# Kernel tuning notes

Hardware: AMD Instinct MI355X
Metric: run time of the kernel (lower is better)

The kernel has to match this reference:

```python
import jax, jax.numpy as jnp
import numpy as np
import math

N = 4096
E = 131072
D_IN = 148      # d_node_feat
D_HID = 128     # d_node_reshape (DIHGNN.d_node_feat)
D_OUT = 148     # d_output


def setup_inputs() -> dict:
    key = jax.random.key(0)
    ks = jax.random.split(key, 10)
    node_feat = jax.random.normal(ks[0], (1, N, D_IN), dtype=jnp.float32)
    edge_index = jax.random.randint(ks[1], (2, E), 0, N, dtype=jnp.int64)
    # learned parameters
    W1 = jax.random.normal(ks[2], (D_HID, D_IN), dtype=jnp.float32) * 0.02
    b1 = jnp.zeros((D_HID,), dtype=jnp.float32)
    a_param = jnp.array([0.9], dtype=jnp.float32)   # DIHGNN.a
    Wd = jax.random.normal(ks[3], (D_OUT, D_HID), dtype=jnp.float32) * 0.02
    bd = jnp.zeros((D_OUT,), dtype=jnp.float32)
    W2 = jax.random.normal(ks[4], (2, D_OUT), dtype=jnp.float32) * 0.02
    b2 = jnp.zeros((2,), dtype=jnp.float32)
    return {"node_feat": node_feat, "edge_index": edge_index, "num_node": N,
            "W1": W1, "b1": b1, "a_param": a_param, "Wd": Wd, "bd": bd,
            "W2": W2, "b2": b2}


def reference(node_feat, edge_index, num_node, W1, b1, a_param, Wd, bd, W2, b2):
    n = num_node
    x = node_feat[0]                                   # [N, D_IN]
    x = x @ W1.T + b1                                  # linear_1 -> [N, D_HID]

    # dense adjacency via scatter-set (duplicates collapse to 1, as in torch)
    adj = jnp.zeros((n, n), dtype=jnp.float32).at[edge_index[0], edge_index[1]].set(1.0)

    # asymmetric degree normalization: D_col^{-1/2} A D_row^{-1/2}
    L = adj.sum(axis=0)                                # column sums
    R = adj.sum(axis=1)                                # row sums
    L_is = jnp.where(L > 0, jax.lax.rsqrt(jnp.maximum(L, 1e-30)), 0.0)
    R_is = jnp.where(R > 0, jax.lax.rsqrt(jnp.maximum(R, 1e-30)), 0.0)
    adj_norm = L_is[:, None] * adj * R_is[None, :]

    # custom tanh: 0.5 + 0.5 * tanh(2 * a)
    alpha = 0.5 + 0.5 * jnp.tanh(2.0 * a_param[0])     # scalar

    # graph diffusion: (I - alpha * A_norm)^{-1} x, as a linear solve
    eye = jnp.eye(n, dtype=jnp.float32)
    x = jnp.linalg.solve(eye - alpha * adj_norm, x)    # [N, D_HID]

    x = x @ Wd.T + bd                                  # DIHGNN.linear -> [N, D_OUT]

    # similarity loss (scaled by DIHGNN.d_node_feat = D_HID)
    sim = (x @ x.T) / math.sqrt(D_HID)                 # [N, N]
    sim = sim * (1.0 - eye)                            # zero diagonal
    sim = jax.nn.relu(sim)
    loss = sim.sum() / (n * (n - 1))

    x = x * (1.0 - alpha)
    x = jax.nn.relu(x)
    pooled = jnp.max(x, axis=0, keepdims=True)         # global_max_pool, single graph -> [1, D_OUT]
    out = pooled @ W2.T + b2                           # [1, 2]
    return (out, loss)
```

## Files before the change

### kernel.cpp

```cpp
#include <hip/hip_runtime.h>
#include <hip/hip_bf16.h>
#include <math.h>

#define N_NODES 4096
#define N_EDGES 131072
#define BCAP 80
#define DIN 148
#define DHID 128
#define DOUT 148
#define KP 160

typedef __attribute__((ext_vector_type(8))) _Float16 half8;
typedef __attribute__((ext_vector_type(4))) float f32x4;

__device__ inline float2 h2f2(unsigned p) {
    union { unsigned u; _Float16 h[2]; } cv; cv.u = p;
    return make_float2((float)cv.h[0], (float)cv.h[1]);
}
__device__ inline unsigned f2h2(float x, float y) {
    union { unsigned u; _Float16 h[2]; } cv;
    cv.h[0] = (_Float16)x; cv.h[1] = (_Float16)y;
    return cv.u;
}
__device__ inline float2 cvtx(unsigned g) { return h2f2(g); }
__device__ inline float2 cvtx(float2 g)   { return g; }

__global__ __launch_bounds__(256) void prep_kernel(const int* __restrict__ ei,
                                                   const float* __restrict__ W1,
                                                   const float* __restrict__ Wd,
                                                   const float* __restrict__ b1,
                                                   const float* __restrict__ nf,
                                                   float* __restrict__ WdT,
                                                   unsigned* __restrict__ bitmap,
                                                   unsigned* __restrict__ bucket,
                                                   int* __restrict__ rowdeg,
                                                   int* __restrict__ coldeg,
                                                   float* __restrict__ Bm,
                                                   unsigned* __restrict__ Bh) {
    int tid = threadIdx.x, bid = blockIdx.x;
    int gtid = bid * 256 + tid;
    if (gtid < DHID * DOUT) {
        int h = gtid / DOUT, o = gtid - h * DOUT;
        WdT[gtid] = Wd[o * DHID + h];
    }
    {
        int i = ei[gtid] & (N_NODES - 1);
        int j = ei[gtid + N_EDGES] & (N_NODES - 1);
        unsigned pos = (unsigned)i * (unsigned)N_NODES + (unsigned)j;
        unsigned w = pos >> 5, m = 1u << (pos & 31u);
        unsigned old = atomicOr(&bitmap[w], m);
        if (!(old & m)) {
            int p = atomicAdd(&rowdeg[i], 1);
            if (p < BCAP) bucket[i * BCAP + p] = (unsigned)j;
            atomicAdd(&coldeg[j], 1);
        }
    }
    __shared__ float sA[16 * 152];
    __shared__ float sB[16 * 128];
    if ((bid & 1) == 0) {
        int r0 = (bid >> 1) * 16;
        for (int idx = tid; idx < 16 * DIN; idx += 256) {
            int nd = idx / DIN, c = idx - nd * DIN;
            sA[nd * 152 + c] = nf[(r0 + nd) * DIN + c];
        }
        __syncthreads();
        int half = tid >> 7, d = tid & 127;
        float a[8];
#pragma unroll
        for (int n = 0; n < 8; ++n) a[n] = 0.f;
        const float* __restrict__ wrow = W1 + d * DIN;
        const float* sb8 = sA + half * 8 * 152;
        for (int kk = 0; kk < DIN; ++kk) {
            float wv = wrow[kk];
#pragma unroll
            for (int n = 0; n < 8; ++n) a[n] += sb8[n * 152 + kk] * wv;
        }
        float bb = b1[d];
#pragma unroll
        for (int n = 0; n < 8; ++n) {
            int nd = half * 8 + n;
            float v = a[n] + bb;
            Bm[(r0 + nd) * DHID + d] = v;
            sB[nd * 128 + d] = v;
        }
        __syncthreads();
        for (int idx = tid; idx < 16 * 64; idx += 256) {
            int nd = idx >> 6, dp = idx & 63;
            Bh[(r0 + nd) * 64 + dp] = f2h2(sB[nd * 128 + 2 * dp], sB[nd * 128 + 2 * dp + 1]);
        }
    }
}

template<bool INH, bool DUAL, bool LAST>
__global__ __launch_bounds__(256) void spmv_kernel(const void* __restrict__ xin_,
                                                   unsigned* __restrict__ xoutH,
                                                   float* __restrict__ xoutF,
                                                   const float* __restrict__ Bm,
                                                   const float* __restrict__ prev2,
                                                   const unsigned* __restrict__ cc,
                                                   const int* __restrict__ rowdeg,
                                                   const int* __restrict__ coldeg,
                                                   const float* __restrict__ a_param,
                                                   double* __restrict__ accd) {
    int tid = threadIdx.x;
    int wid = __builtin_amdgcn_readfirstlane(tid >> 6);
    int lane = tid & 63;
    int r = blockIdx.x * 4 + wid;
    int dg = min(rowdeg[r], BCAP);
    int nch = (dg + 7) >> 3;
    float alpha = 0.5f + 0.5f * tanhf(2.0f * a_param[0]);
    int cdg = coldeg[r];
    float ac = (cdg > 0) ? alpha * rsqrtf((float)cdg) : 0.0f;
    const uint4* __restrict__ q = (const uint4*)(cc + r * BCAP);
    const unsigned* __restrict__ xh = (const unsigned*)xin_;
    const float2* __restrict__ x2f = (const float2*)xin_;
    auto ld = [&](unsigned col) {
        if constexpr (INH) return xh[col * 64 + lane];
        else               return x2f[col * 64 + lane];
    };
    float ax = 0.f, ay = 0.f;
    uint4 ca = q[0], cb = q[1];
    auto g0 = ld(ca.x), g1 = ld(ca.y), g2 = ld(ca.z), g3 = ld(ca.w);
    auto g4 = ld(cb.x), g5 = ld(cb.y), g6 = ld(cb.z), g7 = ld(cb.w);
    int d0 = rowdeg[ca.x], d1 = rowdeg[ca.y], d2 = rowdeg[ca.z], d3 = rowdeg[ca.w];
    int d4 = rowdeg[cb.x], d5 = rowdeg[cb.y], d6 = rowdeg[cb.z], d7 = rowdeg[cb.w];
    uint4 na = q[2], nb = q[3];
    for (int c = 0; c < nch; ++c) {
        auto h0 = ld(na.x), h1 = ld(na.y), h2 = ld(na.z), h3 = ld(na.w);
        auto h4 = ld(nb.x), h5 = ld(nb.y), h6 = ld(nb.z), h7 = ld(nb.w);
        int e0 = rowdeg[na.x], e1 = rowdeg[na.y], e2 = rowdeg[na.z], e3 = rowdeg[na.w];
        int e4 = rowdeg[nb.x], e5 = rowdeg[nb.y], e6 = rowdeg[nb.z], e7 = rowdeg[nb.w];
        uint4 fa = q[2 * c + 4], fb = q[2 * c + 5];
        int t = c * 8;
        float2 x0 = cvtx(g0), x1 = cvtx(g1), x2 = cvtx(g2), x3 = cvtx(g3);
        float2 x4 = cvtx(g4), x5 = cvtx(g5), x6 = cvtx(g6), x7 = cvtx(g7);
        float c0 = (t + 0 < dg && d0 > 0) ? rsqrtf((float)d0) : 0.f;
        float c1 = (t + 1 < dg && d1 > 0) ? rsqrtf((float)d1) : 0.f;
        float c2 = (t + 2 < dg && d2 > 0) ? rsqrtf((float)d2) : 0.f;
        float c3 = (t + 3 < dg && d3 > 0) ? rsqrtf((float)d3) : 0.f;
        float c4 = (t + 4 < dg && d4 > 0) ? rsqrtf((float)d4) : 0.f;
        float c5 = (t + 5 < dg && d5 > 0) ? rsqrtf((float)d5) : 0.f;
        float c6 = (t + 6 < dg && d6 > 0) ? rsqrtf((float)d6) : 0.f;
        float c7 = (t + 7 < dg && d7 > 0) ? rsqrtf((float)d7) : 0.f;
        ax += c0 * x0.x + c1 * x1.x + c2 * x2.x + c3 * x3.x
            + c4 * x4.x + c5 * x5.x + c6 * x6.x + c7 * x7.x;
        ay += c0 * x0.y + c1 * x1.y + c2 * x2.y + c3 * x3.y
            + c4 * x4.y + c5 * x5.y + c6 * x6.y + c7 * x7.y;
        g0 = h0; g1 = h1; g2 = h2; g3 = h3;
        g4 = h4; g5 = h5; g6 = h6; g7 = h7;
        d0 = e0; d1 = e1; d2 = e2; d3 = e3;
        d4 = e4; d5 = e5; d6 = e6; d7 = e7;
        na = fa; nb = fb;
    }
    int idx = r * 64 + lane;
    float2 b = ((const float2*)Bm)[idx];
    float vx = b.x + ac * ax, vy = b.y + ac * ay;
    if constexpr (LAST) {
        ((float2*)xoutF)[idx] = make_float2(vx, vy);
        float2 xp = x2f[idx];
        float2 p2 = ((const float2*)prev2)[idx];
        float dpx = xp.x - p2.x, dpy = xp.y - p2.y;
        float dnx = vx - xp.x, dny = vy - xp.y;
        double s0 = (double)dpx * dpx + (double)dpy * dpy;
        double s1 = (double)dnx * dpx + (double)dny * dpy;
        __shared__ double sh0[256], sh1[256];
        sh0[tid] = s0; sh1[tid] = s1;
        __syncthreads();
        for (int off = 128; off > 0; off >>= 1) {
            if (tid < off) { sh0[tid] += sh0[tid + off]; sh1[tid] += sh1[tid + off]; }
            __syncthreads();
        }
        if (tid == 0) { atomicAdd(&accd[1], sh0[0]); atomicAdd(&accd[2], sh1[0]); }
    } else {
        xoutH[idx] = f2h2(vx, vy);
        if constexpr (DUAL) ((float2*)xoutF)[idx] = make_float2(vx, vy);
    }
}

__global__ __launch_bounds__(256) void post_kernel(const float* __restrict__ last,
                                                   const float* __restrict__ prev,
                                                   const double* __restrict__ accd,
                                                   const float* __restrict__ WdT,
                                                   const float* __restrict__ bd,
                                                   _Float16* __restrict__ yH,
                                                   unsigned* __restrict__ mcolu) {
    int tid = threadIdx.x, bid = blockIdx.x;
    int r0 = bid * 16;
    double d0 = accd[1], d1 = accd[2];
    float lam = (d0 > 0.0) ? (float)(d1 / d0) : 0.0f;
    float den = 1.0f - lam;
    if (fabsf(den) < 1e-4f) den = (den < 0.0f) ? -1e-4f : 1e-4f;
    float sf = fminf(fmaxf(lam / den, -1e4f), 1e4f);
    __shared__ float sx[16 * DHID];
    for (int idx = tid; idx < 16 * DHID; idx += 256) {
        int node = r0 + (idx >> 7), ccol = idx & 127;
        float l = last[node * DHID + ccol];
        sx[idx] = l + sf * (l - prev[node * DHID + ccol]);
    }
    __syncthreads();
    for (int idx = tid; idx < 16 * (KP - DOUT); idx += 256) {
        int node = r0 + idx / (KP - DOUT);
        int ccol = DOUT + idx % (KP - DOUT);
        yH[node * KP + ccol] = (_Float16)0.0f;
    }
    if (tid < DOUT) {
        float acc[16];
#pragma unroll
        for (int nd = 0; nd < 16; ++nd) acc[nd] = 0.f;
        for (int h = 0; h < DHID; ++h) {
            float wv = WdT[h * DOUT + tid];
#pragma unroll
            for (int nd = 0; nd < 16; ++nd) acc[nd] += sx[nd * DHID + h] * wv;
        }
        float bb = bd[tid];
        float lm = 0.0f;
#pragma unroll
        for (int nd = 0; nd < 16; ++nd) {
            float v = acc[nd] + bb;
            yH[(r0 + nd) * KP + tid] = (_Float16)v;
            lm = fmaxf(lm, v);
        }
        atomicMax(&mcolu[tid], __float_as_uint(lm));
    }
}

__global__ __launch_bounds__(256) void simloss_kernel(const _Float16* __restrict__ yH,
                                                      double* __restrict__ accd,
                                                      unsigned* __restrict__ cnt,
                                                      const unsigned* __restrict__ mcolu,
                                                      const float* __restrict__ W2,
                                                      const float* __restrict__ b2,
                                                      const float* __restrict__ a_param,
                                                      float* __restrict__ out) {
    int tid = threadIdx.x;
    int tb = blockIdx.x;
    int ti = 0, rem = tb;
    while (rem >= 32 - ti) { rem -= 32 - ti; ++ti; }
    int tj = ti + rem;
    int wid = tid >> 6, lane = tid & 63;
    int wr = wid >> 1, wc = wid & 1;
    int fr = lane & 15, kq = lane >> 4;
    const half8* __restrict__ ap =
        (const half8*)(yH + (size_t)(ti * 128 + wr * 64 + fr) * KP);
    const half8* __restrict__ bp =
        (const half8*)(yH + (size_t)(tj * 128 + wc * 64 + fr) * KP);
    f32x4 C[4][4];
#pragma unroll
    for (int m = 0; m < 4; ++m)
#pragma unroll
        for (int n = 0; n < 4; ++n) C[m][n] = (f32x4)0.0f;
#pragma unroll
    for (int kk = 0; kk < KP / 32; ++kk) {
        half8 a[4], bf[4];
#pragma unroll
        for (int m = 0; m < 4; ++m) a[m] = ap[m * 320 + kk * 4 + kq];
#pragma unroll
        for (int n = 0; n < 4; ++n) bf[n] = bp[n * 320 + kk * 4 + kq];
#pragma unroll
        for (int m = 0; m < 4; ++m)
#pragma unroll
            for (int n = 0; n < 4; ++n)
                C[m][n] = __builtin_amdgcn_mfma_f32_16x16x32_f16(a[m], bf[n], C[m][n], 0, 0, 0);
    }
    const float inv = 0.0883883476483184405f;
    float wgt = (ti == tj) ? 1.0f : 2.0f;
    float lsum = 0.0f;
    int rq = kq * 4;
#pragma unroll
    for (int m = 0; m < 4; ++m)
#pragma unroll
        for (int n = 0; n < 4; ++n)
#pragma unroll
            for (int reg = 0; reg < 4; ++reg) {
                int gi = ti * 128 + wr * 64 + m * 16 + rq + reg;
                int gj = tj * 128 + wc * 64 + n * 16 + fr;
                float v = C[m][n][reg] * inv;
                if (gi != gj && v > 0.0f) lsum += wgt * v;
            }
    for (int o2 = 32; o2 > 0; o2 >>= 1) lsum += __shfl_down(lsum, o2);
    __shared__ float ws[4];
    __shared__ bool lastblk;
    if ((tid & 63) == 0) ws[tid >> 6] = lsum;
    __syncthreads();
    if (tid == 0) {
        atomicAdd(&accd[0], (double)(ws[0] + ws[1] + ws[2] + ws[3]));
        __threadfence();
        unsigned r = __hip_atomic_fetch_add(&cnt[1], 1u, __ATOMIC_ACQ_REL,
                                            __HIP_MEMORY_SCOPE_AGENT);
        lastblk = (r == 527u);
    }
    __syncthreads();
    if (lastblk && tid < 64) {
        float alpha = 0.5f + 0.5f * tanhf(2.0f * a_param[0]);
        float oma = 1.0f - alpha;
        float s0 = 0.0f, s1 = 0.0f;
        for (int o = tid; o < DOUT; o += 64) {
            float p = __uint_as_float(mcolu[o]);
            s0 += p * W2[o];
            s1 += p * W2[DOUT + o];
        }
        for (int off = 32; off > 0; off >>= 1) {
            s0 += __shfl_down(s0, off);
            s1 += __shfl_down(s1, off);
        }
        if (tid == 0) {
            double loss = __hip_atomic_load(&accd[0], __ATOMIC_RELAXED,
                                            __HIP_MEMORY_SCOPE_AGENT);
            out[0] = b2[0] + oma * s0;
            out[1] = b2[1] + oma * s1;
            out[2] = (float)(loss / (4096.0 * 4095.0));
        }
    }
}

extern "C" void kernel_launch(void* const* d_in, const int* in_sizes, int n_in,
                              void* d_out, int out_size, void* d_ws, size_t ws_size,
                              hipStream_t stream) {
    (void)in_sizes; (void)n_in; (void)out_size; (void)ws_size;
    const float* node_feat  = (const float*)d_in[0];
    const int*   edge_index = (const int*)d_in[1];
    const float* W1         = (const float*)d_in[3];
    const float* b1         = (const float*)d_in[4];
    const float* a_param    = (const float*)d_in[5];
    const float* Wd         = (const float*)d_in[6];
    const float* bd         = (const float*)d_in[7];
    const float* W2         = (const float*)d_in[8];
    const float* b2         = (const float*)d_in[9];
    float*       out        = (float*)d_out;

    char* w = (char*)d_ws;
    size_t off = 0;
    auto alloc = [&](size_t bytes) -> char* {
        char* p = w + off;
        off = (off + bytes + 255) & ~(size_t)255;
        return p;
    };
    double*   accd    = (double*)   alloc(8 * sizeof(double));
    unsigned* cnt     = (unsigned*) alloc(16 * sizeof(unsigned));
    int*      rowdeg  = (int*)      alloc(N_NODES * 4);
    int*      coldeg  = (int*)      alloc(N_NODES * 4);
    unsigned* mcolu   = (unsigned*) alloc(256 * 4);
    unsigned* bitmap  = (unsigned*) alloc((size_t)N_NODES * N_NODES / 8);
    unsigned* bucket  = (unsigned*) alloc((size_t)N_NODES * BCAP * 4 + 1024);
    size_t zero_end = off;
    float*    WdT     = (float*)    alloc(DHID * DOUT * 4);
    float*    Bm      = (float*)    alloc(N_NODES * DHID * 4);
    unsigned* Bh      = (unsigned*) alloc((size_t)N_NODES * 64 * 4);
    unsigned* H0      = (unsigned*) alloc((size_t)N_NODES * 64 * 4);
    unsigned* H1      = (unsigned*) alloc((size_t)N_NODES * 64 * 4);
    float*    Y0      = (float*)    alloc(N_NODES * DHID * 4);
    float*    Y1      = (float*)    alloc(N_NODES * DHID * 4);
    float*    Y2      = (float*)    alloc(N_NODES * DHID * 4);
    _Float16* yH      = (_Float16*) alloc((size_t)N_NODES * KP * 2);

    hipMemsetAsync(w, 0, zero_end, stream);

    prep_kernel<<<N_EDGES / 256, 256, 0, stream>>>(edge_index, W1, Wd, b1, node_feat,
                                                   WdT, bitmap, bucket, rowdeg, coldeg,
                                                   Bm, Bh);

    const int GB = N_NODES / 4;
    spmv_kernel<true,  false, false><<<GB, 256, 0, stream>>>(Bh, H0, nullptr, Bm, nullptr, bucket, rowdeg, coldeg, a_param, accd);
    spmv_kernel<true,  false, false><<<GB, 256, 0, stream>>>(H0, H1, nullptr, Bm, nullptr, bucket, rowdeg, coldeg, a_param, accd);
    spmv_kernel<true,  false, false><<<GB, 256, 0, stream>>>(H1, H0, nullptr, Bm, nullptr, bucket, rowdeg, coldeg, a_param, accd);
    spmv_kernel<true,  true,  false><<<GB, 256, 0, stream>>>(H0, H1, Y0, Bm, nullptr, bucket, rowdeg, coldeg, a_param, accd);
    spmv_kernel<true,  true,  false><<<GB, 256, 0, stream>>>(H1, H0, Y1, Bm, nullptr, bucket, rowdeg, coldeg, a_param, accd);
    spmv_kernel<false, false, true ><<<GB, 256, 0, stream>>>(Y1, nullptr, Y2, Bm, Y0, bucket, rowdeg, coldeg, a_param, accd);

    post_kernel<<<N_NODES / 16, 256, 0, stream>>>(Y2, Y1, accd, WdT, bd, yH, mcolu);
    simloss_kernel<<<528, 256, 0, stream>>>(yH, accd, cnt, mcolu, W2, b2, a_param, out);
}
```

Before: 166.4 us.

## Replace sparse gather SpMV iterations with dense fp16 MFMA GEMM over materialized adjacency

Materializes the normalized adjacency as a dense 4096x4096 fp16 matrix and runs each diffusion iteration as a dense MFMA GEMM against a transposed feature matrix, replacing the gather-based SpMV. The state layout changes to feature-major (transposed), and the prep and post kernels are adapted to match. This gives up sparsity: each iteration now streams 32 MB of mostly zeros and does about 100x more FLOPs, in exchange for regular coalesced loads and matrix cores. Each 16-row block re-reads its whole A slice with little reuse.

After: 400.6 us. 141% more time.

```diff
diff --git a/kernel.cpp b/kernel.cpp
--- a/kernel.cpp
+++ b/kernel.cpp
@@ -12,18 +12,6 @@
 
 typedef __attribute__((ext_vector_type(8))) _Float16 half8;
 typedef __attribute__((ext_vector_type(4))) float f32x4;
-
-__device__ inline float2 h2f2(unsigned p) {
-    union { unsigned u; _Float16 h[2]; } cv; cv.u = p;
-    return make_float2((float)cv.h[0], (float)cv.h[1]);
-}
-__device__ inline unsigned f2h2(float x, float y) {
-    union { unsigned u; _Float16 h[2]; } cv;
-    cv.h[0] = (_Float16)x; cv.h[1] = (_Float16)y;
-    return cv.u;
-}
-__device__ inline float2 cvtx(unsigned g) { return h2f2(g); }
-__device__ inline float2 cvtx(float2 g)   { return g; }
 
 __global__ __launch_bounds__(256) void prep_kernel(const int* __restrict__ ei,
                                                    const float* __restrict__ W1,
@@ -35,8 +23,8 @@
                                                    unsigned* __restrict__ bucket,
                                                    int* __restrict__ rowdeg,
                                                    int* __restrict__ coldeg,
-                                                   float* __restrict__ Bm,
-                                                   unsigned* __restrict__ Bh) {
+                                                   float* __restrict__ BT,
+                                                   _Float16* __restrict__ XT0) {
     int tid = threadIdx.x, bid = blockIdx.x;
     int gtid = bid * 256 + tid;
     if (gtid < DHID * DOUT) {
@@ -77,92 +65,91 @@
         }
         float bb = b1[d];
 #pragma unroll
-        for (int n = 0; n < 8; ++n) {
-            int nd = half * 8 + n;
-            float v = a[n] + bb;
-            Bm[(r0 + nd) * DHID + d] = v;
-            sB[nd * 128 + d] = v;
-        }
+        for (int n = 0; n < 8; ++n)
+            sB[(half * 8 + n) * 128 + d] = a[n] + bb;
         __syncthreads();
-        for (int idx = tid; idx < 16 * 64; idx += 256) {
-            int nd = idx >> 6, dp = idx & 63;
-            Bh[(r0 + nd) * 64 + dp] = f2h2(sB[nd * 128 + 2 * dp], sB[nd * 128 + 2 * dp + 1]);
-        }
-    }
-}
-
-template<bool INH, bool DUAL, bool LAST>
-__global__ __launch_bounds__(256) void spmv_kernel(const void* __restrict__ xin_,
-                                                   unsigned* __restrict__ xoutH,
-                                                   float* __restrict__ xoutF,
-                                                   const float* __restrict__ Bm,
-                                                   const float* __restrict__ prev2,
-                                                   const unsigned* __restrict__ cc,
-                                                   const int* __restrict__ rowdeg,
-                                                   const int* __restrict__ coldeg,
-                                                   const float* __restrict__ a_param,
+        for (int idx = tid; idx < 16 * DHID; idx += 256) {
+            int ff = idx >> 4, nd = idx & 15;
+            float v = sB[nd * 128 + ff];
+            BT[(size_t)ff * N_NODES + r0 + nd] = v;
+            XT0[(size_t)ff * N_NODES + r0 + nd] = (_Float16)v;
+        }
+    }
+}
+
+__global__ __launch_bounds__(256) void buildA_kernel(const unsigned* __restrict__ bucket,
+                                                     const int* __restrict__ rowdeg,
+                                                     const int* __restrict__ coldeg,
+                                                     const float* __restrict__ a_param,
+                                                     _Float16* __restrict__ Ah) {
+    int wv = threadIdx.x >> 6, lane = threadIdx.x & 63;
+    int r = blockIdx.x * 4 + wv;
+    uint4* rowp = (uint4*)(Ah + (size_t)r * N_NODES);
+#pragma unroll
+    for (int t = 0; t < 8; ++t)
+        rowp[t * 64 + lane] = make_uint4(0u, 0u, 0u, 0u);
+    asm volatile("s_waitcnt vmcnt(0)" ::: "memory");
+    int dg = min(rowdeg[r], BCAP);
+    float alpha = 0.5f + 0.5f * tanhf(2.0f * a_param[0]);
+    int cd = coldeg[r];
+    float ac = (cd > 0) ? alpha * rsqrtf((float)cd) : 0.0f;
+    for (int q = lane; q < dg; q += 64) {
+        unsigned col = bucket[r * BCAP + q];
+        int rd = rowdeg[col];
+        float rsj = (rd > 0) ? rsqrtf((float)rd) : 0.0f;
+        Ah[(size_t)r * N_NODES + col] = (_Float16)(ac * rsj);
+    }
+}
+
+template<bool DUAL, bool LAST>
+__global__ __launch_bounds__(256) void gemm_kernel(const _Float16* __restrict__ Ah,
+                                                   const _Float16* __restrict__ Xin,
+                                                   _Float16* __restrict__ Xout,
+                                                   const float* __restrict__ BT,
+                                                   float* __restrict__ XF,
+                                                   const float* __restrict__ XFp,
+                                                   const float* __restrict__ XFpp,
                                                    double* __restrict__ accd) {
-    int tid = threadIdx.x;
-    int wid = __builtin_amdgcn_readfirstlane(tid >> 6);
-    int lane = tid & 63;
-    int r = blockIdx.x * 4 + wid;
-    int dg = min(rowdeg[r], BCAP);
-    int nch = (dg + 7) >> 3;
-    float alpha = 0.5f + 0.5f * tanhf(2.0f * a_param[0]);
-    int cdg = coldeg[r];
-    float ac = (cdg > 0) ? alpha * rsqrtf((float)cdg) : 0.0f;
-    const uint4* __restrict__ q = (const uint4*)(cc + r * BCAP);
-    const unsigned* __restrict__ xh = (const unsigned*)xin_;
-    const float2* __restrict__ x2f = (const float2*)xin_;
-    auto ld = [&](unsigned col) {
-        if constexpr (INH) return xh[col * 64 + lane];
-        else               return x2f[col * 64 + lane];
-    };
-    float ax = 0.f, ay = 0.f;
-    uint4 ca = q[0], cb = q[1];
-    auto g0 = ld(ca.x), g1 = ld(ca.y), g2 = ld(ca.z), g3 = ld(ca.w);
-    auto g4 = ld(cb.x), g5 = ld(cb.y), g6 = ld(cb.z), g7 = ld(cb.w);
-    int d0 = rowdeg[ca.x], d1 = rowdeg[ca.y], d2 = rowdeg[ca.z], d3 = rowdeg[ca.w];
-    int d4 = rowdeg[cb.x], d5 = rowdeg[cb.y], d6 = rowdeg[cb.z], d7 = rowdeg[cb.w];
-    uint4 na = q[2], nb = q[3];
-    for (int c = 0; c < nch; ++c) {
-        auto h0 = ld(na.x), h1 = ld(na.y), h2 = ld(na.z), h3 = ld(na.w);
-        auto h4 = ld(nb.x), h5 = ld(nb.y), h6 = ld(nb.z), h7 = ld(nb.w);
-        int e0 = rowdeg[na.x], e1 = rowdeg[na.y], e2 = rowdeg[na.z], e3 = rowdeg[na.w];
-        int e4 = rowdeg[nb.x], e5 = rowdeg[nb.y], e6 = rowdeg[nb.z], e7 = rowdeg[nb.w];
-        uint4 fa = q[2 * c + 4], fb = q[2 * c + 5];
-        int t = c * 8;
-        float2 x0 = cvtx(g0), x1 = cvtx(g1), x2 = cvtx(g2), x3 = cvtx(g3);
-        float2 x4 = cvtx(g4), x5 = cvtx(g5), x6 = cvtx(g6), x7 = cvtx(g7);
-        float c0 = (t + 0 < dg && d0 > 0) ? rsqrtf((float)d0) : 0.f;
-        float c1 = (t + 1 < dg && d1 > 0) ? rsqrtf((float)d1) : 0.f;
-        float c2 = (t + 2 < dg && d2 > 0) ? rsqrtf((float)d2) : 0.f;
-        float c3 = (t + 3 < dg && d3 > 0) ? rsqrtf((float)d3) : 0.f;
-        float c4 = (t + 4 < dg && d4 > 0) ? rsqrtf((float)d4) : 0.f;
-        float c5 = (t + 5 < dg && d5 > 0) ? rsqrtf((float)d5) : 0.f;
-        float c6 = (t + 6 < dg && d6 > 0) ? rsqrtf((float)d6) : 0.f;
-        float c7 = (t + 7 < dg && d7 > 0) ? rsqrtf((float)d7) : 0.f;
-        ax += c0 * x0.x + c1 * x1.x + c2 * x2.x + c3 * x3.x
-            + c4 * x4.x + c5 * x5.x + c6 * x6.x + c7 * x7.x;
-        ay += c0 * x0.y + c1 * x1.y + c2 * x2.y + c3 * x3.y
-            + c4 * x4.y + c5 * x5.y + c6 * x6.y + c7 * x7.y;
-        g0 = h0; g1 = h1; g2 = h2; g3 = h3;
-        g4 = h4; g5 = h5; g6 = h6; g7 = h7;
-        d0 = e0; d1 = e1; d2 = e2; d3 = e3;
-        d4 = e4; d5 = e5; d6 = e6; d7 = e7;
-        na = fa; nb = fb;
-    }
-    int idx = r * 64 + lane;
-    float2 b = ((const float2*)Bm)[idx];
-    float vx = b.x + ac * ax, vy = b.y + ac * ay;
+    int tid = threadIdx.x, bid = blockIdx.x;
+    int I0 = bid * 16;
+    int wv = tid >> 6, lane = tid & 63;
+    int n0 = wv * 32;
+    int fr = lane & 15, kq = lane >> 4;
+    const half8* __restrict__ ap  = (const half8*)(Ah  + (size_t)(I0 + fr) * N_NODES);
+    const half8* __restrict__ bp0 = (const half8*)(Xin + (size_t)(n0 + fr) * N_NODES);
+    const half8* __restrict__ bp1 = (const half8*)(Xin + (size_t)(n0 + 16 + fr) * N_NODES);
+    f32x4 acc0 = (f32x4)0.0f, acc1 = (f32x4)0.0f;
+#pragma unroll 4
+    for (int kk = 0; kk < N_NODES / 32; ++kk) {
+        half8 a  = ap[kk * 4 + kq];
+        half8 b0 = bp0[kk * 4 + kq];
+        half8 b1 = bp1[kk * 4 + kq];
+        acc0 = __builtin_amdgcn_mfma_f32_16x16x32_f16(a, b0, acc0, 0, 0, 0);
+        acc1 = __builtin_amdgcn_mfma_f32_16x16x32_f16(a, b1, acc1, 0, 0, 0);
+    }
+    double s0 = 0.0, s1 = 0.0;
+#pragma unroll
+    for (int j = 0; j < 2; ++j) {
+        const f32x4& A = j ? acc1 : acc0;
+#pragma unroll
+        for (int reg = 0; reg < 4; ++reg) {
+            int gi = I0 + kq * 4 + reg;
+            int gj = n0 + j * 16 + fr;
+            int idx = gj * N_NODES + gi;
+            float vx = BT[idx] + A[reg];
+            if constexpr (!LAST) Xout[idx] = (_Float16)vx;
+            if constexpr (DUAL || LAST) XF[idx] = vx;
+            if constexpr (LAST) {
+                float xp = XFp[idx];
+                float p2 = XFpp[idx];
+                float dp = xp - p2;
+                float dn = vx - xp;
+                s0 += (double)dp * (double)dp;
+                s1 += (double)dn * (double)dp;
+            }
+        }
+    }
     if constexpr (LAST) {
-        ((float2*)xoutF)[idx] = make_float2(vx, vy);
-        float2 xp = x2f[idx];
-        float2 p2 = ((const float2*)prev2)[idx];
-        float dpx = xp.x - p2.x, dpy = xp.y - p2.y;
-        float dnx = vx - xp.x, dny = vy - xp.y;
-        double s0 = (double)dpx * dpx + (double)dpy * dpy;
-        double s1 = (double)dnx * dpx + (double)dny * dpy;
         __shared__ double sh0[256], sh1[256];
         sh0[tid] = s0; sh1[tid] = s1;
         __syncthreads();
@@ -171,9 +158,6 @@
             __syncthreads();
         }
         if (tid == 0) { atomicAdd(&accd[1], sh0[0]); atomicAdd(&accd[2], sh1[0]); }
-    } else {
-        xoutH[idx] = f2h2(vx, vy);
-        if constexpr (DUAL) ((float2*)xoutF)[idx] = make_float2(vx, vy);
     }
 }
 
@@ -193,9 +177,10 @@
     float sf = fminf(fmaxf(lam / den, -1e4f), 1e4f);
     __shared__ float sx[16 * DHID];
     for (int idx = tid; idx < 16 * DHID; idx += 256) {
-        int node = r0 + (idx >> 7), ccol = idx & 127;
-        float l = last[node * DHID + ccol];
-        sx[idx] = l + sf * (l - prev[node * DHID + ccol]);
+        int ff = idx >> 4, nd = idx & 15;
+        float l = last[(size_t)ff * N_NODES + r0 + nd];
+        float p = prev[(size_t)ff * N_NODES + r0 + nd];
+        sx[nd * DHID + ff] = l + sf * (l - p);
     }
     __syncthreads();
     for (int idx = tid; idx < 16 * (KP - DOUT); idx += 256) {
@@ -341,32 +326,32 @@
     int*      coldeg  = (int*)      alloc(N_NODES * 4);
     unsigned* mcolu   = (unsigned*) alloc(256 * 4);
     unsigned* bitmap  = (unsigned*) alloc((size_t)N_NODES * N_NODES / 8);
-    unsigned* bucket  = (unsigned*) alloc((size_t)N_NODES * BCAP * 4 + 1024);
     size_t zero_end = off;
+    unsigned* bucket  = (unsigned*) alloc((size_t)N_NODES * BCAP * 4);
     float*    WdT     = (float*)    alloc(DHID * DOUT * 4);
-    float*    Bm      = (float*)    alloc(N_NODES * DHID * 4);
-    unsigned* Bh      = (unsigned*) alloc((size_t)N_NODES * 64 * 4);
-    unsigned* H0      = (unsigned*) alloc((size_t)N_NODES * 64 * 4);
-    unsigned* H1      = (unsigned*) alloc((size_t)N_NODES * 64 * 4);
-    float*    Y0      = (float*)    alloc(N_NODES * DHID * 4);
-    float*    Y1      = (float*)    alloc(N_NODES * DHID * 4);
-    float*    Y2      = (float*)    alloc(N_NODES * DHID * 4);
+    float*    BT      = (float*)    alloc((size_t)DHID * N_NODES * 4);
+    _Float16* Ah      = (_Float16*) alloc((size_t)N_NODES * N_NODES * 2);
+    _Float16* XTa     = (_Float16*) alloc((size_t)DHID * N_NODES * 2);
+    _Float16* XTb     = (_Float16*) alloc((size_t)DHID * N_NODES * 2);
+    float*    XF4     = (float*)    alloc((size_t)DHID * N_NODES * 4);
+    float*    XF5     = (float*)    alloc((size_t)DHID * N_NODES * 4);
+    float*    XF6     = (float*)    alloc((size_t)DHID * N_NODES * 4);
     _Float16* yH      = (_Float16*) alloc((size_t)N_NODES * KP * 2);
 
     hipMemsetAsync(w, 0, zero_end, stream);
 
     prep_kernel<<<N_EDGES / 256, 256, 0, stream>>>(edge_index, W1, Wd, b1, node_feat,
                                                    WdT, bitmap, bucket, rowdeg, coldeg,
-                                                   Bm, Bh);
-
-    const int GB = N_NODES / 4;
-    spmv_kernel<true,  false, false><<<GB, 256, 0, stream>>>(Bh, H0, nullptr, Bm, nullptr, bucket, rowdeg, coldeg, a_param, accd);
-    spmv_kernel<true,  false, false><<<GB, 256, 0, stream>>>(H0, H1, nullptr, Bm, nullptr, bucket, rowdeg, coldeg, a_param, accd);
-    spmv_kernel<true,  false, false><<<GB, 256, 0, stream>>>(H1, H0, nullptr, Bm, nullptr, bucket, rowdeg, coldeg, a_param, accd);
-    spmv_kernel<true,  true,  false><<<GB, 256, 0, stream>>>(H0, H1, Y0, Bm, nullptr, bucket, rowdeg, coldeg, a_param, accd);
-    spmv_kernel<true,  true,  false><<<GB, 256, 0, stream>>>(H1, H0, Y1, Bm, nullptr, bucket, rowdeg, coldeg, a_param, accd);
-    spmv_kernel<false, false, true ><<<GB, 256, 0, stream>>>(Y1, nullptr, Y2, Bm, Y0, bucket, rowdeg, coldeg, a_param, accd);
-
-    post_kernel<<<N_NODES / 16, 256, 0, stream>>>(Y2, Y1, accd, WdT, bd, yH, mcolu);
+                                                   BT, XTa);
+    buildA_kernel<<<N_NODES / 4, 256, 0, stream>>>(bucket, rowdeg, coldeg, a_param, Ah);
+
+    gemm_kernel<false, false><<<256, 256, 0, stream>>>(Ah, XTa, XTb, BT, nullptr, nullptr, nullptr, accd);
+    gemm_kernel<false, false><<<256, 256, 0, stream>>>(Ah, XTb, XTa, BT, nullptr, nullptr, nullptr, accd);
+    gemm_kernel<false, false><<<256, 256, 0, stream>>>(Ah, XTa, XTb, BT, nullptr, nullptr, nullptr, accd);
+    gemm_kernel<true,  false><<<256, 256, 0, stream>>>(Ah, XTb, XTa, BT, XF4, nullptr, nullptr, accd);
+    gemm_kernel<true,  false><<<256, 256, 0, stream>>>(Ah, XTa, XTb, BT, XF5, nullptr, nullptr, accd);
+    gemm_kernel<false, true ><<<256, 256, 0, stream>>>(Ah, XTb, nullptr, BT, XF6, XF5, XF4, accd);
+
+    post_kernel<<<N_NODES / 16, 256, 0, stream>>>(XF6, XF5, accd, WdT, bd, yH, mcolu);
     simloss_kernel<<<528, 256, 0, stream>>>(yH, accd, cnt, mcolu, W2, b2, a_param, out);
 }
```
